# Optimization experiments

Measured on AMD Instinct MI355X. Metric: run time of the kernel, lower is better.

Reference implementation:

```python
import math
import jax, jax.numpy as jnp
import numpy as np

S, B, H, L, V = 1024, 8, 1024, 6, 32000
FF = 4 * H

def setup_inputs() -> dict:
    key = jax.random.key(0)
    ks = jax.random.split(key, 16)
    w = lambda k, shape: (jax.random.normal(k, shape, jnp.float32) * 0.02)
    return {
        'src': jax.random.randint(ks[0], (S, B), 0, V, dtype=jnp.int32),
        'src_mask': jnp.ones((S, B), dtype=bool),
        'emb': w(ks[1], (V, H)),
        'Wq': w(ks[2], (L, H, H)), 'bq': w(ks[3], (L, H)),
        'Wk': w(ks[4], (L, H, H)), 'bk': w(ks[5], (L, H)),
        'Wv': w(ks[6], (L, H, H)), 'bv': w(ks[7], (L, H)),
        'Wo': w(ks[8], (L, H, H)), 'bo': w(ks[9], (L, H)),
        'W1': w(ks[10], (L, H, FF)), 'b1': w(ks[11], (L, FF)),
        'W2': w(ks[12], (L, FF, H)), 'b2': w(ks[13], (L, H)),
        'g1': jnp.ones((L, H)), 'be1': jnp.zeros((L, H)),
        'g2': jnp.ones((L, H)), 'be2': jnp.zeros((L, H)),
        'gf': jnp.ones((H,)), 'bf': jnp.zeros((H,)),
    }

def _ln(x, g, b, eps=1e-5):
    m = x.mean(-1, keepdims=True)
    v = ((x - m) ** 2).mean(-1, keepdims=True)
    return (x - m) / jnp.sqrt(v + eps) * g + b

def _pos_encoding(seq_len, d):
    pos = jnp.arange(seq_len, dtype=jnp.float32)[:, None]
    div = jnp.exp(jnp.arange(0, d, 2, dtype=jnp.float32) * (-math.log(10000.0) / d))
    pe = jnp.zeros((seq_len, d), jnp.float32)
    pe = pe.at[:, 0::2].set(jnp.sin(pos * div)).at[:, 1::2].set(jnp.cos(pos * div))
    return pe

def reference(src, src_mask, emb, Wq, bq, Wk, bk, Wv, bv, Wo, bo,
              W1, b1, W2, b2, g1, be1, g2, be2, gf, bf):
    Ss, Bs = src.shape
    Hd = emb.shape[1]
    scale = math.sqrt(Hd)
    pe = _pos_encoding(Ss, Hd)
    x = emb[src] * scale + pe[:, None, :]        # (S, B, H)
    key_mask = src_mask.T                         # (B, S_key); mask repeated over query dim
    neg = jnp.asarray(-1e9, x.dtype)

    def step(x, p):
        wq, bq_, wk, bk_, wv, bv_, wo, bo_, w1, b1_, w2, b2_, g1_, be1_, g2_, be2_ = p
        q = (jnp.einsum('sbh,hd->sbd', x, wq) + bq_) / scale
        k = jnp.einsum('sbh,hd->sbd', x, wk) + bk_
        v = jnp.einsum('sbh,hd->sbd', x, wv) + bv_
        scores = jnp.einsum('qbd,kbd->bqk', q, k)            # (B, Sq, Sk)
        scores = jnp.where(key_mask[:, None, :], scores, neg)
        p_attn = jax.nn.softmax(scores, axis=-1)
        ctx = jnp.einsum('bqk,kbd->qbd', p_attn, v)          # (S, B, H)
        src2 = jnp.einsum('sbh,hd->sbd', ctx, wo) + bo_
        x = _ln(x + src2, g1_, be1_)
        ff = jax.nn.relu(jnp.einsum('sbh,hf->sbf', x, w1) + b1_)
        ff = jnp.einsum('sbf,fh->sbh', ff, w2) + b2_
        x = _ln(x + ff, g2_, be2_)
        return x, None

    x, _ = jax.lax.scan(step, x, (Wq, bq, Wk, bk, Wv, bv, Wo, bo,
                                  W1, b1, W2, b2, g1, be1, g2, be2))
    return _ln(x, gf, bf)
```

## Files before the change

kernel.cpp:

```cpp
#include <hip/hip_runtime.h>
#include <cstdint>
#include <cmath>

typedef _Float16 f16;
typedef _Float16 f16x4 __attribute__((ext_vector_type(4)));
typedef _Float16 f16x8 __attribute__((ext_vector_type(8)));
typedef float f32x4 __attribute__((ext_vector_type(4)));

static constexpr int S_ = 1024, B_ = 8, H_ = 1024, L_ = 6, FF_ = 4096;
static constexpr int SBr = S_ * B_;

__device__ __forceinline__ void gload16(const f16* g, f16* l)
{
  __builtin_amdgcn_global_load_lds(
      (const __attribute__((address_space(1))) void*)g,
      (__attribute__((address_space(3))) void*)l,
      16, 0, 0);
}

__global__ __launch_bounds__(256) void gemm_bt_kernel(
    const f16* __restrict__ A, int lda, long long sAb,
    const f16* __restrict__ BT, int ldb, long long sBb,
    f16* __restrict__ C, int ldc, long long sCb,
    int M, int N, int K,
    const float* __restrict__ bias, float alpha, int doRelu, int transC, int ldct)
{
  __shared__ __align__(16) f16 sm[2][2][128 * 32];

  const int t  = threadIdx.x;
  const int wv = t >> 6, ln = t & 63;
  const int wm = wv >> 1, wn = wv & 1;
  const int q4 = ln >> 4, l15 = ln & 15;

  const int nx = gridDim.x, ny = gridDim.y;
  const int nwg = nx * ny * gridDim.z;
  int lin = blockIdx.x + nx * (blockIdx.y + ny * blockIdx.z);
  if ((nwg & 7) == 0)
    lin = (lin & 7) * (nwg >> 3) + (lin >> 3);
  const int bz  = lin / (nx * ny);
  const int rem = lin - bz * nx * ny;
  const int by  = rem / nx;
  const int bx  = rem - by * nx;
  const int tm = by * 128, tn = bx * 128;

  A  += (long long)bz * sAb;
  BT += (long long)bz * sBb;
  C  += (long long)bz * sCb;

  const int ar = (wv << 4) + (ln >> 2);
  const int ac = (ln & 3) * 8;
  const f16* gA0 = A  + (size_t)(tm + ar) * lda + ac;
  const f16* gA1 = gA0 + (size_t)64 * lda;
  const f16* gB0 = BT + (size_t)(tn + ar) * ldb + ac;
  const f16* gB1 = gB0 + (size_t)64 * ldb;
  const int sOff = wv * 512;

  f32x4 acc[4][4];
#pragma unroll
  for (int i = 0; i < 4; ++i)
#pragma unroll
    for (int j = 0; j < 4; ++j)
      acc[i][j] = (f32x4){0.f, 0.f, 0.f, 0.f};

  gload16(gA0, &sm[0][0][sOff]);
  gload16(gA1, &sm[0][0][sOff + 2048]);
  gload16(gB0, &sm[0][1][sOff]);
  gload16(gB1, &sm[0][1][sOff + 2048]);
  __syncthreads();

  int cur = 0;
  for (int kt = 0; kt < K; kt += 32) {
    const int nxt = cur ^ 1;
    if (kt + 32 < K) {
      gload16(gA0 + kt + 32, &sm[nxt][0][sOff]);
      gload16(gA1 + kt + 32, &sm[nxt][0][sOff + 2048]);
      gload16(gB0 + kt + 32, &sm[nxt][1][sOff]);
      gload16(gB1 + kt + 32, &sm[nxt][1][sOff + 2048]);
    }
    const f16* As = &sm[cur][0][0];
    const f16* Bs = &sm[cur][1][0];

    f16x8 af[4], bfr[4];
#pragma unroll
    for (int mi = 0; mi < 4; ++mi)
      af[mi] = *(const f16x8*)(As + (size_t)(wm*64 + mi*16 + l15) * 32 + q4 * 8);
#pragma unroll
    for (int ni = 0; ni < 4; ++ni)
      bfr[ni] = *(const f16x8*)(Bs + (size_t)(wn*64 + ni*16 + l15) * 32 + q4 * 8);
#pragma unroll
    for (int mi = 0; mi < 4; ++mi)
#pragma unroll
      for (int ni = 0; ni < 4; ++ni)
        acc[mi][ni] = __builtin_amdgcn_mfma_f32_16x16x32_f16(af[mi], bfr[ni], acc[mi][ni], 0, 0, 0);

    __syncthreads();
    cur = nxt;
  }

#pragma unroll
  for (int ni = 0; ni < 4; ++ni) {
    const int col = tn + wn*64 + ni*16 + l15;
    const float bb = bias ? bias[col] : 0.f;
#pragma unroll
    for (int mi = 0; mi < 4; ++mi) {
#pragma unroll
      for (int r = 0; r < 4; ++r) {
        const int row = tm + wm*64 + mi*16 + q4*4 + r;
        float v = (acc[mi][ni][r] + bb) * alpha;
        if (doRelu) v = fmaxf(v, 0.f);
        if (transC) C[(size_t)col * ldct + row] = (f16)v;
        else        C[(size_t)row * ldc  + col] = (f16)v;
      }
    }
  }
}

__global__ __launch_bounds__(256) void transpose_kernel(
    const float* __restrict__ in, f16* __restrict__ out, int R, int C)
{
  __shared__ f16 tile[32][33];
  const int tx = threadIdx.x & 31, ty = threadIdx.x >> 5;
  const int c0 = blockIdx.x * 32, r0 = blockIdx.y * 32;
#pragma unroll
  for (int j = 0; j < 32; j += 8)
    tile[ty + j][tx] = (f16)in[(size_t)(r0 + ty + j) * C + c0 + tx];
  __syncthreads();
#pragma unroll
  for (int j = 0; j < 32; j += 8)
    out[(size_t)(c0 + ty + j) * R + r0 + tx] = tile[tx][ty + j];
}

__global__ __launch_bounds__(256) void embed_kernel(
    const int* __restrict__ src, const float* __restrict__ emb, f16* __restrict__ x)
{
  const int r = blockIdx.x;
  const int s = r >> 3;
  const int tok = src[r];
  const float kdiv = -9.2103403719761836e0f / (float)H_;
  for (int h = threadIdx.x; h < H_; h += 256) {
    const float div = expf((float)(h & ~1) * kdiv);
    const float a = (float)s * div;
    const float pe = (h & 1) ? cosf(a) : sinf(a);
    x[(size_t)r * H_ + h] = (f16)(emb[(size_t)tok * H_ + h] * 32.0f + pe);
  }
}

__global__ __launch_bounds__(256) void softmax_kernel(f16* P)
{
  f16* p = P + (size_t)blockIdx.x * 1024;
  const int t = threadIdx.x, wv = t >> 6, ln = t & 63;
  __shared__ float sred[4];
  f16x4 hv = *(const f16x4*)(p + t * 4);
  float v[4];
  float mx = -1e30f;
#pragma unroll
  for (int i = 0; i < 4; ++i) { v[i] = (float)hv[i]; mx = fmaxf(mx, v[i]); }
  for (int off = 32; off; off >>= 1) mx = fmaxf(mx, __shfl_down(mx, off));
  if (ln == 0) sred[wv] = mx;
  __syncthreads();
  mx = fmaxf(fmaxf(sred[0], sred[1]), fmaxf(sred[2], sred[3]));
  float sum = 0.f;
#pragma unroll
  for (int i = 0; i < 4; ++i) { v[i] = __expf(v[i] - mx); sum += v[i]; }
  for (int off = 32; off; off >>= 1) sum += __shfl_down(sum, off);
  __syncthreads();
  if (ln == 0) sred[wv] = sum;
  __syncthreads();
  const float inv = 1.0f / (sred[0] + sred[1] + sred[2] + sred[3]);
#pragma unroll
  for (int i = 0; i < 4; ++i) hv[i] = (f16)(v[i] * inv);
  *(f16x4*)(p + t * 4) = hv;
}

__global__ __launch_bounds__(256) void add_ln_kernel(
    const f16* x, const f16* rr, const float* g, const float* be,
    f16* outH, float* outF)
{
  const size_t row = blockIdx.x;
  const f16* px = x + row * H_;
  const f16* pr = rr ? rr + row * H_ : nullptr;
  const int t = threadIdx.x, wv = t >> 6, ln = t & 63;
  const int h0 = t * 4;
  __shared__ float sred[4];
  float v[4], s = 0.f;
  const f16x4 xv = *(const f16x4*)(px + h0);
  f16x4 rv;
  if (pr) rv = *(const f16x4*)(pr + h0);
#pragma unroll
  for (int i = 0; i < 4; ++i) {
    float a = (float)xv[i];
    if (pr) a += (float)rv[i];
    v[i] = a; s += a;
  }
  for (int off = 32; off; off >>= 1) s += __shfl_down(s, off);
  if (ln == 0) sred[wv] = s;
  __syncthreads();
  const float mean = (sred[0] + sred[1] + sred[2] + sred[3]) * (1.0f / H_);
  float s2 = 0.f;
#pragma unroll
  for (int i = 0; i < 4; ++i) { const float d = v[i] - mean; s2 += d * d; }
  for (int off = 32; off; off >>= 1) s2 += __shfl_down(s2, off);
  __syncthreads();
  if (ln == 0) sred[wv] = s2;
  __syncthreads();
  const float var = (sred[0] + sred[1] + sred[2] + sred[3]) * (1.0f / H_);
  const float inv = 1.0f / sqrtf(var + 1e-5f);
  const float4 gv = *(const float4*)(g + h0);
  const float4 bv = *(const float4*)(be + h0);
  float o[4];
#pragma unroll
  for (int i = 0; i < 4; ++i)
    o[i] = (v[i] - mean) * inv * ((const float*)&gv)[i] + ((const float*)&bv)[i];
  if (outF) {
    *(float4*)(outF + row * H_ + h0) = (float4){o[0], o[1], o[2], o[3]};
  } else {
    f16x4 ov;
#pragma unroll
    for (int i = 0; i < 4; ++i) ov[i] = (f16)o[i];
    *(f16x4*)(outH + row * H_ + h0) = ov;
  }
}


static void gemm_bt(hipStream_t st,
                    const f16* A, int lda, long long sAb,
                    const f16* BT, int ldb, long long sBb,
                    f16* C, int ldc, long long sCb,
                    int M, int N, int K, int nb,
                    const float* bias, float alpha, int relu, int transC, int ldct)
{
  dim3 grid(N / 128, M / 128, nb);
  gemm_bt_kernel<<<grid, dim3(256), 0, st>>>(A, lda, sAb, BT, ldb, sBb,
                                             C, ldc, sCb, M, N, K,
                                             bias, alpha, relu, transC, ldct);
}

extern "C" void kernel_launch(void* const* d_in, const int* in_sizes, int n_in,
                              void* d_out, int out_size, void* d_ws, size_t ws_size,
                              hipStream_t stream)
{
  const int*   src = (const int*)d_in[0];
  const float* emb = (const float*)d_in[2];
  const float* Wq  = (const float*)d_in[3];
  const float* bq  = (const float*)d_in[4];
  const float* Wk  = (const float*)d_in[5];
  const float* bk  = (const float*)d_in[6];
  const float* Wv  = (const float*)d_in[7];
  const float* bv  = (const float*)d_in[8];
  const float* Wo  = (const float*)d_in[9];
  const float* bo  = (const float*)d_in[10];
  const float* W1  = (const float*)d_in[11];
  const float* b1  = (const float*)d_in[12];
  const float* W2  = (const float*)d_in[13];
  const float* b2  = (const float*)d_in[14];
  const float* g1  = (const float*)d_in[15];
  const float* be1 = (const float*)d_in[16];
  const float* g2  = (const float*)d_in[17];
  const float* be2 = (const float*)d_in[18];
  const float* gf  = (const float*)d_in[19];
  const float* bfv = (const float*)d_in[20];

  const size_t E  = (size_t)SBr * H_;
  const size_t HH = (size_t)H_ * H_;
  const size_t HF = (size_t)H_ * FF_;
  const size_t need = (9 * E + E + E / 2) * sizeof(f16);
  if (ws_size < need) return;

  f16* ws  = (f16*)d_ws;
  f16* x   = ws;
  f16* q   = ws + 1*E;
  f16* k   = ws + 2*E;
  f16* vT  = ws + 3*E;
  f16* tmp = ws + 4*E;
  f16* ff  = ws + 5*E;
  f16* P   = ff;
  f16* wT  = ws + 9*E;
  f16* wTq = wT;
  f16* wTk = wT + 1*HH;
  f16* wTv = wT + 2*HH;
  f16* wTo = wT + 3*HH;
  f16* wT1 = wT + 4*HH;
  f16* wT2 = wT + 4*HH + HF;

  const dim3 blk(256);
  embed_kernel<<<SBr, blk, 0, stream>>>(src, emb, x);

  for (int l = 0; l < L_; ++l) {
    const float *Wq_l = Wq + (size_t)l * HH, *Wk_l = Wk + (size_t)l * HH;
    const float *Wv_l = Wv + (size_t)l * HH, *Wo_l = Wo + (size_t)l * HH;
    const float *W1_l = W1 + (size_t)l * HF, *W2_l = W2 + (size_t)l * HF;
    const float *bq_l = bq + (size_t)l * H_, *bk_l = bk + (size_t)l * H_;
    const float *bv_l = bv + (size_t)l * H_, *bo_l = bo + (size_t)l * H_;
    const float *b1_l = b1 + (size_t)l * FF_, *b2_l = b2 + (size_t)l * H_;

    transpose_kernel<<<dim3(H_/32,  H_/32), blk, 0, stream>>>(Wq_l, wTq, H_,  H_);
    transpose_kernel<<<dim3(H_/32,  H_/32), blk, 0, stream>>>(Wk_l, wTk, H_,  H_);
    transpose_kernel<<<dim3(H_/32,  H_/32), blk, 0, stream>>>(Wv_l, wTv, H_,  H_);
    transpose_kernel<<<dim3(H_/32,  H_/32), blk, 0, stream>>>(Wo_l, wTo, H_,  H_);
    transpose_kernel<<<dim3(FF_/32, H_/32), blk, 0, stream>>>(W1_l, wT1, H_,  FF_);
    transpose_kernel<<<dim3(H_/32, FF_/32), blk, 0, stream>>>(W2_l, wT2, FF_, H_);

    gemm_bt(stream, x, H_, 0, wTq, H_, 0, q, H_, 0, SBr, H_, H_, 1,
            bq_l, 1.0f/32.0f, 0, 0, 0);
    gemm_bt(stream, x, H_, 0, wTk, H_, 0, k, H_, 0, SBr, H_, H_, 1,
            bk_l, 1.0f, 0, 0, 0);
    gemm_bt(stream, x, B_*H_, H_, wTv, H_, 0, vT, 0, (long long)HH, S_, H_, H_, B_,
            bv_l, 1.0f, 0, 1, S_);
    gemm_bt(stream, q, B_*H_, H_, k, B_*H_, H_, P, S_, (long long)S_*S_,
            S_, S_, H_, B_, nullptr, 1.0f, 0, 0, 0);
    softmax_kernel<<<B_*S_, blk, 0, stream>>>(P);
    gemm_bt(stream, P, S_, (long long)S_*S_, vT, S_, (long long)HH,
            q, B_*H_, H_, S_, H_, S_, B_, nullptr, 1.0f, 0, 0, 0);
    gemm_bt(stream, q, H_, 0, wTo, H_, 0, tmp, H_, 0, SBr, H_, H_, 1,
            bo_l, 1.0f, 0, 0, 0);
    add_ln_kernel<<<SBr, blk, 0, stream>>>(x, tmp, g1 + (size_t)l*H_, be1 + (size_t)l*H_, x, nullptr);
    gemm_bt(stream, x, H_, 0, wT1, H_, 0, ff, FF_, 0, SBr, FF_, H_, 1,
            b1_l, 1.0f, 1, 0, 0);
    gemm_bt(stream, ff, FF_, 0, wT2, FF_, 0, tmp, H_, 0, SBr, H_, FF_, 1,
            b2_l, 1.0f, 0, 0, 0);
    add_ln_kernel<<<SBr, blk, 0, stream>>>(x, tmp, g2 + (size_t)l*H_, be2 + (size_t)l*H_, x, nullptr);
  }

  add_ln_kernel<<<SBr, blk, 0, stream>>>(x, nullptr, gf, bfv, nullptr, (float*)d_out);
}
```

Measured before the change: 2.653 ms.

## Enlarge GEMM tile to 128x256 with BK=64, swizzled LDS, and explicit waitcnt pipelining

The fp16 MFMA GEMM kernel moves from 4 waves on a 128x128x32 tile to 8 waves on a 128x256x64 tile. Each wave still computes a 64x64 output block. LDS tiles are XOR-swizzled on 16-byte chunks to reduce bank conflicts. The double-buffered k-loop now uses raw s_barrier and s_waitcnt vmcnt so the prefetch of the next stage overlaps compute, and s_setprio is raised around the MFMA block. The aim is fewer global loads per FLOP, fewer barriers per k-step and better latency hiding. The cost is 96KB of LDS per block, fewer resident blocks, and a requirement that N be a multiple of 256.

```diff
diff --git a/kernel.cpp b/kernel.cpp
--- a/kernel.cpp
+++ b/kernel.cpp
@@ -18,18 +18,19 @@
       16, 0, 0);
 }
 
-__global__ __launch_bounds__(256) void gemm_bt_kernel(
+__global__ __launch_bounds__(512) void gemm_bt_kernel(
     const f16* __restrict__ A, int lda, long long sAb,
     const f16* __restrict__ BT, int ldb, long long sBb,
     f16* __restrict__ C, int ldc, long long sCb,
     int M, int N, int K,
     const float* __restrict__ bias, float alpha, int doRelu, int transC, int ldct)
 {
-  __shared__ __align__(16) f16 sm[2][2][128 * 32];
+  __shared__ __align__(16) f16 sA[2][128 * 64];
+  __shared__ __align__(16) f16 sB[2][256 * 64];
 
   const int t  = threadIdx.x;
   const int wv = t >> 6, ln = t & 63;
-  const int wm = wv >> 1, wn = wv & 1;
+  const int wm = wv >> 2, wn = wv & 3;
   const int q4 = ln >> 4, l15 = ln & 15;
 
   const int nx = gridDim.x, ny = gridDim.y;
@@ -41,19 +42,17 @@
   const int rem = lin - bz * nx * ny;
   const int by  = rem / nx;
   const int bx  = rem - by * nx;
-  const int tm = by * 128, tn = bx * 128;
+  const int tm = by * 128, tn = bx * 256;
 
   A  += (long long)bz * sAb;
   BT += (long long)bz * sBb;
   C  += (long long)bz * sCb;
 
-  const int ar = (wv << 4) + (ln >> 2);
-  const int ac = (ln & 3) * 8;
-  const f16* gA0 = A  + (size_t)(tm + ar) * lda + ac;
-  const f16* gA1 = gA0 + (size_t)64 * lda;
-  const f16* gB0 = BT + (size_t)(tn + ar) * ldb + ac;
-  const f16* gB1 = gB0 + (size_t)64 * ldb;
-  const int sOff = wv * 512;
+  const int srow = ln >> 3;
+  const int scol = ((ln & 7) ^ srow) * 8;
+  const f16* gA = A  + (size_t)(tm + wv * 8 + srow) * lda + scol;
+  const f16* gB = BT + (size_t)(tn + wv * 8 + srow) * ldb + scol;
+  const int dOff = wv * 512;
 
   f32x4 acc[4][4];
 #pragma unroll
@@ -62,40 +61,63 @@
     for (int j = 0; j < 4; ++j)
       acc[i][j] = (f32x4){0.f, 0.f, 0.f, 0.f};
 
-  gload16(gA0, &sm[0][0][sOff]);
-  gload16(gA1, &sm[0][0][sOff + 2048]);
-  gload16(gB0, &sm[0][1][sOff]);
-  gload16(gB1, &sm[0][1][sOff + 2048]);
-  __syncthreads();
+  const int ra = wm * 64 + l15;
+  const int rb = wn * 64 + l15;
+  const int x7 = l15 & 7;
+
+#define STAGE(buf, kt) do {                                                   \
+    gload16(gA + (kt),                        &sA[buf][dOff]);                \
+    gload16(gA + (kt) + (size_t)64  * lda,    &sA[buf][dOff + 4096]);         \
+    gload16(gB + (kt),                        &sB[buf][dOff]);                \
+    gload16(gB + (kt) + (size_t)64  * ldb,    &sB[buf][dOff + 4096]);         \
+    gload16(gB + (kt) + (size_t)128 * ldb,    &sB[buf][dOff + 8192]);         \
+    gload16(gB + (kt) + (size_t)192 * ldb,    &sB[buf][dOff + 12288]);        \
+  } while (0)
+
+  STAGE(0, 0);
 
   int cur = 0;
-  for (int kt = 0; kt < K; kt += 32) {
-    const int nxt = cur ^ 1;
-    if (kt + 32 < K) {
-      gload16(gA0 + kt + 32, &sm[nxt][0][sOff]);
-      gload16(gA1 + kt + 32, &sm[nxt][0][sOff + 2048]);
-      gload16(gB0 + kt + 32, &sm[nxt][1][sOff]);
-      gload16(gB1 + kt + 32, &sm[nxt][1][sOff + 2048]);
+  for (int kt = 0; kt < K; kt += 64) {
+    asm volatile("" ::: "memory");
+    __builtin_amdgcn_s_barrier();
+    asm volatile("" ::: "memory");
+    if (kt + 64 < K) {
+      STAGE(cur ^ 1, kt + 64);
+      asm volatile("s_waitcnt vmcnt(6)" ::: "memory");
+    } else {
+      asm volatile("s_waitcnt vmcnt(0)" ::: "memory");
     }
-    const f16* As = &sm[cur][0][0];
-    const f16* Bs = &sm[cur][1][0];
-
-    f16x8 af[4], bfr[4];
-#pragma unroll
-    for (int mi = 0; mi < 4; ++mi)
-      af[mi] = *(const f16x8*)(As + (size_t)(wm*64 + mi*16 + l15) * 32 + q4 * 8);
-#pragma unroll
-    for (int ni = 0; ni < 4; ++ni)
-      bfr[ni] = *(const f16x8*)(Bs + (size_t)(wn*64 + ni*16 + l15) * 32 + q4 * 8);
-#pragma unroll
-    for (int mi = 0; mi < 4; ++mi)
-#pragma unroll
-      for (int ni = 0; ni < 4; ++ni)
-        acc[mi][ni] = __builtin_amdgcn_mfma_f32_16x16x32_f16(af[mi], bfr[ni], acc[mi][ni], 0, 0, 0);
-
-    __syncthreads();
-    cur = nxt;
-  }
+    __builtin_amdgcn_s_barrier();
+    asm volatile("" ::: "memory");
+
+    const f16* As = sA[cur];
+    const f16* Bs = sB[cur];
+
+    f16x8 bfr[4][2];
+#pragma unroll
+    for (int n = 0; n < 4; ++n)
+#pragma unroll
+      for (int ks = 0; ks < 2; ++ks)
+        bfr[n][ks] = *(const f16x8*)(Bs + (size_t)(rb + n*16) * 64
+                                        + (((ks*4 + q4) ^ x7) * 8));
+
+    __builtin_amdgcn_s_setprio(1);
+#pragma unroll
+    for (int m = 0; m < 4; ++m) {
+      const f16x8 a0 = *(const f16x8*)(As + (size_t)(ra + m*16) * 64
+                                          + (((    q4) ^ x7) * 8));
+      const f16x8 a1 = *(const f16x8*)(As + (size_t)(ra + m*16) * 64
+                                          + (((4 + q4) ^ x7) * 8));
+#pragma unroll
+      for (int n = 0; n < 4; ++n) {
+        acc[m][n] = __builtin_amdgcn_mfma_f32_16x16x32_f16(a0, bfr[n][0], acc[m][n], 0, 0, 0);
+        acc[m][n] = __builtin_amdgcn_mfma_f32_16x16x32_f16(a1, bfr[n][1], acc[m][n], 0, 0, 0);
+      }
+    }
+    __builtin_amdgcn_s_setprio(0);
+    cur ^= 1;
+  }
+#undef STAGE
 
 #pragma unroll
   for (int ni = 0; ni < 4; ++ni) {
@@ -229,8 +251,8 @@
                     int M, int N, int K, int nb,
                     const float* bias, float alpha, int relu, int transC, int ldct)
 {
-  dim3 grid(N / 128, M / 128, nb);
-  gemm_bt_kernel<<<grid, dim3(256), 0, st>>>(A, lda, sAb, BT, ldb, sBb,
+  dim3 grid(N / 256, M / 128, nb);
+  gemm_bt_kernel<<<grid, dim3(512), 0, st>>>(A, lda, sAb, BT, ldb, sBb,
                                              C, ldc, sCb, M, N, K,
                                              bias, alpha, relu, transC, ldct);
 }
```

Result: slower. 2.807 ms (+5.8%).
